# Performance work log

Hardware: AMD Instinct MI355X
Metric: run time of the kernel (lower is better)

The kernel has to match this reference:

```python
import jax, jax.numpy as jnp
import numpy as np

N_NODES = 100000
N_EDGES = 1600000
B = 256
H = 512
HEADS = 8
DH = H // HEADS


def setup_inputs() -> dict:
    key = jax.random.key(0)
    ks = list(jax.random.split(key, 24))
    def nrm(i, shape, s=0.02):
        return jax.random.normal(ks[i], shape, jnp.float32) * s
    inp = {}
    inp["text_features"] = jax.random.normal(ks[0], (B, 768), jnp.float32)
    inp["video_features"] = jax.random.normal(ks[1], (B, 512), jnp.float32)
    inp["x"] = jax.random.normal(ks[2], (N_NODES, 64), jnp.float32)
    inp["edge_index"] = jax.random.randint(ks[3], (2, N_EDGES), 0, N_NODES, dtype=jnp.int32)
    # sorted node->graph assignment covering all B graphs (no empty segments)
    inp["batch_idx"] = ((jnp.arange(N_NODES) * B) // N_NODES).astype(jnp.int32)
    inp["Wt"] = nrm(4, (768, H)); inp["bt"] = jnp.zeros((H,), jnp.float32)
    inp["Wv"] = nrm(5, (512, H)); inp["bv"] = jnp.zeros((H,), jnp.float32)
    inp["Wq"] = nrm(6, (H, H)); inp["bq"] = jnp.zeros((H,), jnp.float32)
    inp["Wk"] = nrm(7, (H, H)); inp["bk"] = jnp.zeros((H,), jnp.float32)
    inp["Wva"] = nrm(8, (H, H)); inp["bva"] = jnp.zeros((H,), jnp.float32)
    inp["Wo"] = nrm(9, (H, H)); inp["bo"] = jnp.zeros((H,), jnp.float32)
    inp["Wf"] = nrm(10, (2 * H, H)); inp["bf"] = jnp.zeros((H,), jnp.float32)
    inp["G1W"] = nrm(11, (64, 128)); inp["G1b"] = jnp.zeros((128,), jnp.float32)
    inp["G2W"] = nrm(12, (128, 128)); inp["G2b"] = jnp.zeros((128,), jnp.float32)
    inp["G3W"] = nrm(13, (128, 256)); inp["G3b"] = jnp.zeros((256,), jnp.float32)
    inp["Wff"] = nrm(14, (H + 256, H)); inp["bff"] = jnp.zeros((H,), jnp.float32)
    inp["Wb"] = nrm(15, (H, 2)); inp["bb"] = jnp.zeros((2,), jnp.float32)
    inp["Wa"] = nrm(16, (H, 2)); inp["ba"] = jnp.zeros((2,), jnp.float32)
    return inp


def _gcn_conv(h, W, b, src, dst, dis):
    # PyG GCNConv: linear transform, symmetric-normalized aggregation w/ self-loops, bias
    hw = h @ W                                       # [N, C]
    norm = dis[src] * dis[dst]                       # [E]
    msg = hw[src] * norm[:, None]                    # [E, C]
    agg = jax.ops.segment_sum(msg, dst, num_segments=h.shape[0])
    agg = agg + hw * (dis * dis)[:, None]            # self-loop messages
    return agg + b


def reference(text_features, video_features, x, edge_index, batch_idx, Wt, bt, Wv, bv, Wq, bq, Wk, bk, Wva, bva, Wo, bo, Wf, bf, G1W, G1b, G2W, G2b, G3W, G3b, Wff, bff, Wb, bb, Wa, ba):
    # encoders (dropout is eval-mode no-op)
    text_enc = jax.nn.relu(text_features @ Wt + bt)      # [B, H]
    video_enc = jax.nn.relu(video_features @ Wv + bv)    # [B, H]
    # multihead attention; torch seq lens are both 1 (batch acts as N)
    q = (text_enc @ Wq + bq).reshape(B, HEADS, 1, DH)
    k = (video_enc @ Wk + bk).reshape(B, HEADS, 1, DH)
    v = (video_enc @ Wva + bva).reshape(B, HEADS, 1, DH)
    scores = jnp.einsum('bhqd,bhkd->bhqk', q, k) / np.float32(np.sqrt(DH))
    w = jax.nn.softmax(scores, axis=-1)
    attn = jnp.einsum('bhqk,bhkd->bhqd', w, v).reshape(B, H)
    text_attended = attn @ Wo + bo
    # multimodal fusion
    fused = jax.nn.relu(jnp.concatenate([text_attended, video_enc], axis=1) @ Wf + bf)
    # GCN stack
    src, dst = edge_index[0], edge_index[1]
    deg = jax.ops.segment_sum(jnp.ones((N_EDGES,), jnp.float32), dst, num_segments=N_NODES) + 1.0
    dis = jax.lax.rsqrt(deg)
    h = jax.nn.elu(_gcn_conv(x, G1W, G1b, src, dst, dis))
    h = jax.nn.elu(_gcn_conv(h, G2W, G2b, src, dst, dis))
    h = _gcn_conv(h, G3W, G3b, src, dst, dis)            # [N, 256]
    # per-graph mean pooling (the original per-batch Python loop, as one segment-mean)
    counts = jax.ops.segment_sum(jnp.ones((N_NODES,), jnp.float32), batch_idx, num_segments=B)
    pooled = jax.ops.segment_sum(h, batch_idx, num_segments=B) / counts[:, None]  # [B, 256]
    # final fusion + classifier heads
    final = jax.nn.relu(jnp.concatenate([fused, pooled], axis=1) @ Wff + bff)
    bullying = jax.nn.log_softmax(final @ Wb + bb, axis=1)
    aggression = jax.nn.log_softmax(final @ Wa + ba, axis=1)
    return bullying, aggression
```

## Files before the change

### kernel.cpp

```cpp
#include <hip/hip_runtime.h>
#include <hip/hip_bf16.h>

#define N_NODES 100000
#define NPAD    100096
#define N_EDGES 1600000
#define BATCH   256
#define HDIM    512

typedef unsigned short u16;
typedef __attribute__((ext_vector_type(8))) short bf16x8;
typedef __attribute__((ext_vector_type(8))) unsigned short u16x8;
typedef __attribute__((ext_vector_type(4))) float f32x4;

__device__ __forceinline__ float bf2f(u16 u) {
    union { unsigned i; float f; } v; v.i = ((unsigned)u) << 16; return v.f;
}
__device__ __forceinline__ u16 f2bf(float f) {
    __hip_bfloat16 h = __float2bfloat16(f);
    return *reinterpret_cast<u16*>(&h);
}

template<int K, int ACT, int SCALE>
__global__ __launch_bounds__(256) void gemm_mfma(
        const u16* __restrict__ A, const u16* __restrict__ Wt,
        const float* __restrict__ bias, const float* __restrict__ dis,
        u16* __restrict__ C, int N) {
    constexpr int RB = K * 2;
    __shared__ u16 As[128 * K];
    __shared__ u16 Bs[128 * K];
    const int tid  = threadIdx.x;
    const int lane = tid & 63;
    const int w    = tid >> 6;
    const int wr   = w >> 1, wc = w & 1;
    const int row0 = blockIdx.y * 128;
    const int col0 = blockIdx.x * 128;

    constexpr int WB     = 128 * RB / 4;
    constexpr int PASSES = WB / 1024;
    const size_t Abase = (size_t)row0 * K;
    const size_t Bbase = (size_t)col0 * K;
    #pragma unroll
    for (int p = 0; p < PASSES; ++p) {
        int Lb  = w * WB + p * 1024;
        int L   = Lb + lane * 16;
        int row = L / RB;
        int cb  = L % RB;
        int scb = cb ^ ((row & 7) << 4);
        const u16* ga = A  + Abase + (size_t)row * K + (scb >> 1);
        const u16* gb = Wt + Bbase + (size_t)row * K + (scb >> 1);
        __builtin_amdgcn_global_load_lds((const __attribute__((address_space(1))) void*)ga,
            (__attribute__((address_space(3))) void*)&As[Lb >> 1], 16, 0, 0);
        __builtin_amdgcn_global_load_lds((const __attribute__((address_space(1))) void*)gb,
            (__attribute__((address_space(3))) void*)&Bs[Lb >> 1], 16, 0, 0);
    }
    asm volatile("s_waitcnt vmcnt(0)" ::: "memory");
    __syncthreads();

    const int rl = lane & 15;
    const int kg = lane >> 4;
    f32x4 acc[4][4] = {};
    #pragma unroll
    for (int s = 0; s < K / 32; ++s) {
        bf16x8 af[4], bg[4];
        #pragma unroll
        for (int m = 0; m < 4; ++m) {
            int row = wr * 64 + m * 16 + rl;
            int cb  = s * 64 + kg * 16;
            int scb = cb ^ ((row & 7) << 4);
            af[m] = *(const bf16x8*)&As[(row * RB + scb) >> 1];
        }
        #pragma unroll
        for (int n = 0; n < 4; ++n) {
            int row = wc * 64 + n * 16 + rl;
            int cb  = s * 64 + kg * 16;
            int scb = cb ^ ((row & 7) << 4);
            bg[n] = *(const bf16x8*)&Bs[(row * RB + scb) >> 1];
        }
        #pragma unroll
        for (int m = 0; m < 4; ++m)
            #pragma unroll
            for (int n = 0; n < 4; ++n)
                acc[m][n] = __builtin_amdgcn_mfma_f32_16x16x32_bf16(af[m], bg[n], acc[m][n], 0, 0, 0);
    }

    #pragma unroll
    for (int m = 0; m < 4; ++m) {
        #pragma unroll
        for (int r = 0; r < 4; ++r) {
            int grow = row0 + wr * 64 + m * 16 + kg * 4 + r;
            float ds = SCALE ? dis[grow] : 1.f;
            #pragma unroll
            for (int n = 0; n < 4; ++n) {
                int gcol = col0 + wc * 64 + n * 16 + rl;
                float v = acc[m][n][r] + bias[gcol];
                if (ACT == 2) v = v > 0.f ? v : expm1f(v);
                C[(size_t)grow * N + gcol] = f2bf(v * ds);
            }
        }
    }
}

template<int ACT>
__global__ __launch_bounds__(256) void gemm_loop(
        const u16* __restrict__ A, const u16* __restrict__ Wt,
        const float* __restrict__ bias, u16* __restrict__ C,
        int N, int K, int lda, int ldc) {
    __shared__ u16 As[128 * 64];
    __shared__ u16 Bs[128 * 64];
    const int tid  = threadIdx.x;
    const int lane = tid & 63;
    const int w    = tid >> 6;
    const int wr   = w >> 1, wc = w & 1;
    const int row0 = blockIdx.y * 128;
    const int col0 = blockIdx.x * 128;
    const int rl = lane & 15;
    const int kg = lane >> 4;
    f32x4 acc[4][4] = {};

    for (int k0 = 0; k0 < K; k0 += 64) {
        #pragma unroll
        for (int p = 0; p < 4; ++p) {
            int Lb  = w * 4096 + p * 1024;
            int L   = Lb + lane * 16;
            int row = L >> 7;
            int cb  = L & 127;
            int scb = cb ^ ((row & 7) << 4);
            const u16* ga = A  + (size_t)(row0 + row) * lda + k0 + (scb >> 1);
            const u16* gb = Wt + (size_t)(col0 + row) * K   + k0 + (scb >> 1);
            __builtin_amdgcn_global_load_lds((const __attribute__((address_space(1))) void*)ga,
                (__attribute__((address_space(3))) void*)&As[Lb >> 1], 16, 0, 0);
            __builtin_amdgcn_global_load_lds((const __attribute__((address_space(1))) void*)gb,
                (__attribute__((address_space(3))) void*)&Bs[Lb >> 1], 16, 0, 0);
        }
        asm volatile("s_waitcnt vmcnt(0)" ::: "memory");
        __syncthreads();
        #pragma unroll
        for (int s = 0; s < 2; ++s) {
            bf16x8 af[4], bg[4];
            #pragma unroll
            for (int m = 0; m < 4; ++m) {
                int row = wr * 64 + m * 16 + rl;
                int cb  = s * 64 + kg * 16;
                int scb = cb ^ ((row & 7) << 4);
                af[m] = *(const bf16x8*)&As[(row * 128 + scb) >> 1];
            }
            #pragma unroll
            for (int n = 0; n < 4; ++n) {
                int row = wc * 64 + n * 16 + rl;
                int cb  = s * 64 + kg * 16;
                int scb = cb ^ ((row & 7) << 4);
                bg[n] = *(const bf16x8*)&Bs[(row * 128 + scb) >> 1];
            }
            #pragma unroll
            for (int m = 0; m < 4; ++m)
                #pragma unroll
                for (int n = 0; n < 4; ++n)
                    acc[m][n] = __builtin_amdgcn_mfma_f32_16x16x32_bf16(af[m], bg[n], acc[m][n], 0, 0, 0);
        }
        __syncthreads();
    }

    #pragma unroll
    for (int m = 0; m < 4; ++m) {
        #pragma unroll
        for (int r = 0; r < 4; ++r) {
            int grow = row0 + wr * 64 + m * 16 + kg * 4 + r;
            #pragma unroll
            for (int n = 0; n < 4; ++n) {
                int gcol = col0 + wc * 64 + n * 16 + rl;
                float v = acc[m][n][r] + bias[gcol];
                if (ACT == 1) v = fmaxf(v, 0.f);
                C[(size_t)grow * ldc + gcol] = f2bf(v);
            }
        }
    }
}

template<int K, int N>
__device__ __forceinline__ void tw(const float* __restrict__ W, u16* __restrict__ Wt, int t) {
    int n = t / K, k = t - n * K;
    Wt[t] = f2bf(W[(size_t)k * N + n]);
}

__global__ void prep(const float* __restrict__ G1W, u16* __restrict__ g1wt,
                     const float* __restrict__ G2W, u16* __restrict__ g2wt,
                     const float* __restrict__ Wv,  u16* __restrict__ WvT,
                     const float* __restrict__ Wva, u16* __restrict__ WvaT,
                     const float* __restrict__ Wo,  u16* __restrict__ WoT,
                     const float* __restrict__ Wf,  u16* __restrict__ WfT,
                     const float* __restrict__ video, u16* __restrict__ vidbf) {
    const int bid = blockIdx.x, tid = threadIdx.x;
    if (bid < 32)        { tw<64, 128>  (G1W, g1wt, bid * 256 + tid); }
    else if (bid < 96)   { tw<128, 128> (G2W, g2wt, (bid - 32) * 256 + tid); }
    else if (bid < 1120) { tw<512, 512> (Wv,  WvT,  (bid - 96) * 256 + tid); }
    else if (bid < 2144) { tw<512, 512> (Wva, WvaT, (bid - 1120) * 256 + tid); }
    else if (bid < 3168) { tw<512, 512> (Wo,  WoT,  (bid - 2144) * 256 + tid); }
    else if (bid < 5216) { tw<1024, 512>(Wf,  WfT,  (bid - 3168) * 256 + tid); }
    else { int t = (bid - 5216) * 256 + tid; vidbf[t] = f2bf(video[t]); }
}

__global__ void final_fused(const u16* __restrict__ fusedb,
                            const float* __restrict__ pooled, const float* __restrict__ counts,
                            const float* __restrict__ G3W, const float* __restrict__ G3b,
                            const float* __restrict__ Wff, const float* __restrict__ bff,
                            const float* __restrict__ Wb,  const float* __restrict__ bb,
                            const float* __restrict__ Wa,  const float* __restrict__ ba,
                            float* __restrict__ out) {
    __shared__ float cat[768], fin[512], pp[128];
    __shared__ float rd[4][4];
    const int b = blockIdx.x, tid = threadIdx.x;
    cat[tid] = bf2f(fusedb[b * 512 + tid]);
    cat[tid + 256] = bf2f(fusedb[b * 512 + 256 + tid]);
    float inv = 1.f / counts[b];
    if (tid < 128) pp[tid] = pooled[b * 128 + tid] * inv;
    __syncthreads();
    {
        float s = G3b[tid];
        #pragma unroll 8
        for (int k = 0; k < 128; ++k) s += pp[k] * G3W[k * 256 + tid];
        cat[512 + tid] = s;
    }
    __syncthreads();
    {
        float a0 = bff[tid], a1 = bff[tid + 256];
        #pragma unroll 8
        for (int k = 0; k < 768; ++k) {
            float xv = cat[k];
            a0 += xv * Wff[k * 512 + tid];
            a1 += xv * Wff[k * 512 + tid + 256];
        }
        fin[tid] = fmaxf(a0, 0.f);
        fin[tid + 256] = fmaxf(a1, 0.f);
    }
    __syncthreads();
    float z0 = 0.f, z1 = 0.f, y0 = 0.f, y1 = 0.f;
    for (int k = tid; k < 512; k += 256) {
        float f = fin[k];
        z0 += f * Wb[2 * k];
        z1 += f * Wb[2 * k + 1];
        y0 += f * Wa[2 * k];
        y1 += f * Wa[2 * k + 1];
    }
    #pragma unroll
    for (int off = 32; off > 0; off >>= 1) {
        z0 += __shfl_down(z0, off);
        z1 += __shfl_down(z1, off);
        y0 += __shfl_down(y0, off);
        y1 += __shfl_down(y1, off);
    }
    int ww = tid >> 6;
    if ((tid & 63) == 0) { rd[ww][0] = z0; rd[ww][1] = z1; rd[ww][2] = y0; rd[ww][3] = y1; }
    __syncthreads();
    if (tid == 0) {
        float Z0 = rd[0][0] + rd[1][0] + rd[2][0] + rd[3][0] + bb[0];
        float Z1 = rd[0][1] + rd[1][1] + rd[2][1] + rd[3][1] + bb[1];
        float Y0 = rd[0][2] + rd[1][2] + rd[2][2] + rd[3][2] + ba[0];
        float Y1 = rd[0][3] + rd[1][3] + rd[2][3] + rd[3][3] + ba[1];
        float m = fmaxf(Z0, Z1);
        float l = m + logf(expf(Z0 - m) + expf(Z1 - m));
        out[b * 2 + 0] = Z0 - l;
        out[b * 2 + 1] = Z1 - l;
        float m2 = fmaxf(Y0, Y1);
        float l2 = m2 + logf(expf(Y0 - m2) + expf(Y1 - m2));
        out[512 + b * 2 + 0] = Y0 - l2;
        out[512 + b * 2 + 1] = Y1 - l2;
    }
}

__global__ void deg_slot(const int* __restrict__ dstE, int* __restrict__ deg,
                         int* __restrict__ slot, int E) {
    int e = blockIdx.x * blockDim.x + threadIdx.x;
    if (e < E) slot[e] = atomicAdd(&deg[dstE[e]], 1);
}

__global__ void scan1(const int* __restrict__ in, int* __restrict__ out,
                      int* __restrict__ bsum, float* __restrict__ dis, int n) {
    __shared__ int ts[256];
    const int tid = threadIdx.x;
    const int base = blockIdx.x * 1024;
    int v[4];
    #pragma unroll
    for (int i = 0; i < 4; ++i) {
        int idx = base + tid * 4 + i;
        v[i] = (idx < n) ? in[idx] : 0;
        if (idx < NPAD) dis[idx] = rsqrtf((float)v[i] + 1.f);
    }
    ts[tid] = v[0] + v[1] + v[2] + v[3];
    __syncthreads();
    for (int off = 1; off < 256; off <<= 1) {
        int val = (tid >= off) ? ts[tid - off] : 0;
        __syncthreads();
        ts[tid] += val;
        __syncthreads();
    }
    int run = (tid == 0) ? 0 : ts[tid - 1];
    if (tid == 255) bsum[blockIdx.x] = ts[255];
    #pragma unroll
    for (int i = 0; i < 4; ++i) {
        int idx = base + tid * 4 + i;
        if (idx < n) out[idx] = run;
        run += v[i];
    }
}

__global__ void scan2(int* __restrict__ bsum, int nb) {
    int l = threadIdx.x;
    int a = (l < nb) ? bsum[l] : 0;
    int b = (l + 64 < nb) ? bsum[l + 64] : 0;
    int oa = a, ob = b;
    #pragma unroll
    for (int off = 1; off < 64; off <<= 1) {
        int t = __shfl_up(a, off);
        if (l >= off) a += t;
    }
    int totA = __shfl(a, 63);
    #pragma unroll
    for (int off = 1; off < 64; off <<= 1) {
        int t = __shfl_up(b, off);
        if (l >= off) b += t;
    }
    if (l < nb) bsum[l] = a - oa;
    if (l + 64 < nb) bsum[l + 64] = totA + b - ob;
}

__global__ void scan3(int* __restrict__ out, const int* __restrict__ bsum, int n, int total) {
    int idx = blockIdx.x * 1024 + threadIdx.x * 4;
    int add = bsum[blockIdx.x];
    #pragma unroll
    for (int i = 0; i < 4; ++i)
        if (idx + i < n) out[idx + i] += add;
    if (blockIdx.x == 0 && threadIdx.x == 0) out[n] = total;
}

__global__ void csr_scatter2(const int* __restrict__ srcE, const int* __restrict__ dstE,
                             const int* __restrict__ rowptr, const int* __restrict__ slot,
                             int* __restrict__ csr_src, int E) {
    int e = blockIdx.x * blockDim.x + threadIdx.x;
    if (e >= E) return;
    csr_src[rowptr[dstE[e]] + slot[e]] = srcE[e];
}

__global__ void scale_rows64_bf16(const float* __restrict__ x, const float* __restrict__ dis,
                                  u16* __restrict__ out) {
    int t = blockIdx.x * blockDim.x + threadIdx.x;
    if (t >= N_NODES * 64) return;
    out[t] = f2bf(x[t] * dis[t >> 6]);
}

template<int C>
__global__ void csr_agg_bf16(const u16* __restrict__ Hs, const int* __restrict__ rowptr,
                             const int* __restrict__ csr_src, const float* __restrict__ dis,
                             u16* __restrict__ out) {
    constexpr int LPG = C / 8;
    constexpr int G   = 64 / LPG;
    int node = blockIdx.x * 4 + (threadIdx.x >> 6);
    if (node >= N_NODES) return;
    int lane = threadIdx.x & 63;
    int g  = lane / LPG;
    int cl = lane % LPG;
    int s0 = rowptr[node], s1 = rowptr[node + 1];
    float a[8] = {};
    if (g == 0) {
        u16x8 v = *(const u16x8*)&Hs[(size_t)node * C + cl * 8];
        #pragma unroll
        for (int j = 0; j < 8; ++j) a[j] = bf2f(v[j]);
    }
    int e = s0 + g;
    while (e + G < s1) {
        int sA = csr_src[e], sB = csr_src[e + G];
        u16x8 vA = *(const u16x8*)&Hs[(size_t)sA * C + cl * 8];
        u16x8 vB = *(const u16x8*)&Hs[(size_t)sB * C + cl * 8];
        #pragma unroll
        for (int j = 0; j < 8; ++j) a[j] += bf2f(vA[j]) + bf2f(vB[j]);
        e += 2 * G;
    }
    while (e < s1) {
        int s = csr_src[e];
        u16x8 v = *(const u16x8*)&Hs[(size_t)s * C + cl * 8];
        #pragma unroll
        for (int j = 0; j < 8; ++j) a[j] += bf2f(v[j]);
        e += G;
    }
    #pragma unroll
    for (int m = LPG; m < 64; m <<= 1)
        #pragma unroll
        for (int j = 0; j < 8; ++j) a[j] += __shfl_xor(a[j], m);
    if (g == 0) {
        float dd = dis[node];
        u16x8 o;
        #pragma unroll
        for (int j = 0; j < 8; ++j) o[j] = f2bf(a[j] * dd);
        *(u16x8*)&out[(size_t)node * C + cl * 8] = o;
    }
}

__global__ __launch_bounds__(256) void csr_agg_pool(
        const u16* __restrict__ Hs, const int* __restrict__ rowptr,
        const int* __restrict__ csr_src, const float* __restrict__ dis,
        const int* __restrict__ batch,
        float* __restrict__ pooled, float* __restrict__ counts) {
    __shared__ float bins[2][128];
    __shared__ int cnt[2];
    const int tid = threadIdx.x;
    const int base = blockIdx.x * 16;
    if (tid < 128) { bins[0][tid] = 0.f; bins[1][tid] = 0.f; }
    if (tid < 2) cnt[tid] = 0;
    __syncthreads();
    const int lane = tid & 63;
    const int w = tid >> 6;
    const int g = lane >> 4;
    const int cl = lane & 15;
    const int b0 = batch[base];
    #pragma unroll
    for (int i = 0; i < 4; ++i) {
        const int node = base + w * 4 + i;
        const int s0 = rowptr[node], s1 = rowptr[node + 1];
        float a[8] = {};
        if (g == 0) {
            u16x8 v = *(const u16x8*)&Hs[(size_t)node * 128 + cl * 8];
            #pragma unroll
            for (int j = 0; j < 8; ++j) a[j] = bf2f(v[j]);
        }
        int e = s0 + g;
        while (e + 4 < s1) {
            int sA = csr_src[e], sB = csr_src[e + 4];
            u16x8 vA = *(const u16x8*)&Hs[(size_t)sA * 128 + cl * 8];
            u16x8 vB = *(const u16x8*)&Hs[(size_t)sB * 128 + cl * 8];
            #pragma unroll
            for (int j = 0; j < 8; ++j) a[j] += bf2f(vA[j]) + bf2f(vB[j]);
            e += 8;
        }
        while (e < s1) {
            int s = csr_src[e];
            u16x8 v = *(const u16x8*)&Hs[(size_t)s * 128 + cl * 8];
            #pragma unroll
            for (int j = 0; j < 8; ++j) a[j] += bf2f(v[j]);
            e += 4;
        }
        #pragma unroll
        for (int m = 16; m < 64; m <<= 1)
            #pragma unroll
            for (int j = 0; j < 8; ++j) a[j] += __shfl_xor(a[j], m);
        if (g == 0) {
            int bin = (batch[node] != b0) ? 1 : 0;
            float dd = dis[node];
            #pragma unroll
            for (int j = 0; j < 8; ++j) atomicAdd(&bins[bin][cl * 8 + j], a[j] * dd);
            if (cl == 0) atomicAdd(&cnt[bin], 1);
        }
    }
    __syncthreads();
    int bin = tid >> 7, c = tid & 127;
    if (cnt[bin] > 0) atomicAdd(&pooled[(b0 + bin) * 128 + c], bins[bin][c]);
    if (tid < 2 && cnt[tid] > 0) atomicAdd(&counts[b0 + tid], (float)cnt[tid]);
}

extern "C" void kernel_launch(void* const* d_in, const int* in_sizes, int n_in,
                              void* d_out, int out_size, void* d_ws, size_t ws_size,
                              hipStream_t stream) {
    const float* video = (const float*)d_in[1];
    const float* x     = (const float*)d_in[2];
    const int*   eidx  = (const int*)d_in[3];
    const int*   batch = (const int*)d_in[4];
    const float* Wv  = (const float*)d_in[7],  *bv  = (const float*)d_in[8];
    const float* Wva = (const float*)d_in[13], *bva = (const float*)d_in[14];
    const float* Wo  = (const float*)d_in[15], *bo  = (const float*)d_in[16];
    const float* Wf  = (const float*)d_in[17], *bf  = (const float*)d_in[18];
    const float* G1W = (const float*)d_in[19], *G1b = (const float*)d_in[20];
    const float* G2W = (const float*)d_in[21], *G2b = (const float*)d_in[22];
    const float* G3W = (const float*)d_in[23], *G3b = (const float*)d_in[24];
    const float* Wff = (const float*)d_in[25], *bff = (const float*)d_in[26];
    const float* Wb  = (const float*)d_in[27], *bb  = (const float*)d_in[28];
    const float* Wa  = (const float*)d_in[29], *ba  = (const float*)d_in[30];
    const int* srcE = eidx;
    const int* dstE = eidx + N_EDGES;

    char* wsc = (char*)d_ws;
    size_t off = 0;
    auto alloc = [&](size_t bytes) { char* p = wsc + off; off += (bytes + 255) & ~(size_t)255; return p; };
    u16*   bufA   = (u16*)  alloc((size_t)NPAD * 128 * 2);
    u16*   bufB   = (u16*)  alloc((size_t)NPAD * 128 * 2);
    float* dis    = (float*)alloc(NPAD * 4);
    int*   deg    = (int*)  alloc(NPAD * 4);
    int*   rowptr = (int*)  alloc((N_NODES + 1) * 4);
    int*   slot   = (int*)  alloc((size_t)N_EDGES * 4);
    int*   csrsrc = (int*)  alloc((size_t)N_EDGES * 4);
    int*   bsum   = (int*)  alloc(128 * 4);
    u16*   g1wt   = (u16*)  alloc(128 * 64 * 2);
    u16*   g2wt   = (u16*)  alloc(128 * 128 * 2);
    u16*   WvT    = (u16*)  alloc(512 * 512 * 2);
    u16*   WvaT   = (u16*)  alloc(512 * 512 * 2);
    u16*   WoT    = (u16*)  alloc(512 * 512 * 2);
    u16*   WfT    = (u16*)  alloc(512 * 1024 * 2);
    u16*   vidbf  = (u16*)  alloc(BATCH * 512 * 2);
    u16*   catb   = (u16*)  alloc(BATCH * 1024 * 2);
    u16*   vattnb = (u16*)  alloc(BATCH * 512 * 2);
    u16*   fusedb = (u16*)  alloc(BATCH * 512 * 2);
    float* pooled = (float*)alloc((BATCH * 128 + BATCH) * 4);
    float* counts = pooled + BATCH * 128;

    const int NB = (N_NODES + 1023) / 1024;
    const int aggGrid = (N_NODES + 3) / 4;

    hipMemsetAsync(deg, 0, NPAD * 4, stream);
    hipMemsetAsync(pooled, 0, (BATCH * 128 + BATCH) * 4, stream);
    deg_slot<<<(N_EDGES + 255) / 256, 256, 0, stream>>>(dstE, deg, slot, N_EDGES);
    scan1<<<NB, 256, 0, stream>>>(deg, rowptr, bsum, dis, N_NODES);
    scan2<<<1, 64, 0, stream>>>(bsum, NB);
    scan3<<<NB, 256, 0, stream>>>(rowptr, bsum, N_NODES, N_EDGES);
    csr_scatter2<<<(N_EDGES + 255) / 256, 256, 0, stream>>>(srcE, dstE, rowptr, slot, csrsrc, N_EDGES);

    prep<<<5728, 256, 0, stream>>>(G1W, g1wt, G2W, g2wt, Wv, WvT, Wva, WvaT,
                                   Wo, WoT, Wf, WfT, video, vidbf);

    dim3 feGrid(4, 2);
    gemm_loop<1><<<feGrid, 256, 0, stream>>>(vidbf, WvT, bv, catb + 512, 512, 512, 512, 1024);
    gemm_loop<0><<<feGrid, 256, 0, stream>>>(catb + 512, WvaT, bva, vattnb, 512, 512, 1024, 512);
    gemm_loop<0><<<feGrid, 256, 0, stream>>>(vattnb, WoT, bo, catb, 512, 512, 512, 1024);
    gemm_loop<1><<<feGrid, 256, 0, stream>>>(catb, WfT, bf, fusedb, 512, 1024, 1024, 512);

    scale_rows64_bf16<<<(N_NODES * 64 + 255) / 256, 256, 0, stream>>>(x, dis, bufA);
    csr_agg_bf16<64><<<aggGrid, 256, 0, stream>>>(bufA, rowptr, csrsrc, dis, bufB);
    gemm_mfma<64, 2, 1><<<dim3(1, NPAD / 128), 256, 0, stream>>>(bufB, g1wt, G1b, dis, bufA, 128);
    csr_agg_bf16<128><<<aggGrid, 256, 0, stream>>>(bufA, rowptr, csrsrc, dis, bufB);
    gemm_mfma<128, 2, 1><<<dim3(1, NPAD / 128), 256, 0, stream>>>(bufB, g2wt, G2b, dis, bufA, 128);
    csr_agg_pool<<<N_NODES / 16, 256, 0, stream>>>(bufA, rowptr, csrsrc, dis, batch, pooled, counts);

    final_fused<<<BATCH, 256, 0, stream>>>(fusedb, pooled, counts, G3W, G3b,
                                           Wff, bff, Wb, bb, Wa, ba, (float*)d_out);
}
```

Baseline: 478.2 us.

## Split 128-wide aggregation across two waves and shrink dense GEMM tiles

The 128-channel CSR aggregation and the pooling aggregation now split each node's channels into two 64-wide halves handled by separate waves. Each wave has 8 edge groups instead of 4, so more neighbour gathers are in flight per node and the cross-lane reduction is shallower. The small batch GEMMs use 64x64 tiles in place of 128x128 to launch 32 blocks instead of 8, filling more compute units. The cost is that node index and rowptr loads are duplicated per half, and the smaller GEMM tiles reuse each loaded tile less.

```diff
diff --git a/kernel.cpp b/kernel.cpp
--- a/kernel.cpp
+++ b/kernel.cpp
@@ -101,26 +101,26 @@
 }
 
 template<int ACT>
-__global__ __launch_bounds__(256) void gemm_loop(
+__global__ __launch_bounds__(256) void gemm64(
         const u16* __restrict__ A, const u16* __restrict__ Wt,
         const float* __restrict__ bias, u16* __restrict__ C,
-        int N, int K, int lda, int ldc) {
-    __shared__ u16 As[128 * 64];
-    __shared__ u16 Bs[128 * 64];
+        int K, int lda, int ldc) {
+    __shared__ u16 As[64 * 64];
+    __shared__ u16 Bs[64 * 64];
     const int tid  = threadIdx.x;
     const int lane = tid & 63;
     const int w    = tid >> 6;
     const int wr   = w >> 1, wc = w & 1;
-    const int row0 = blockIdx.y * 128;
-    const int col0 = blockIdx.x * 128;
+    const int row0 = blockIdx.y * 64;
+    const int col0 = blockIdx.x * 64;
     const int rl = lane & 15;
     const int kg = lane >> 4;
-    f32x4 acc[4][4] = {};
+    f32x4 acc[2][2] = {};
 
     for (int k0 = 0; k0 < K; k0 += 64) {
         #pragma unroll
-        for (int p = 0; p < 4; ++p) {
-            int Lb  = w * 4096 + p * 1024;
+        for (int p = 0; p < 2; ++p) {
+            int Lb  = w * 2048 + p * 1024;
             int L   = Lb + lane * 16;
             int row = L >> 7;
             int cb  = L & 127;
@@ -136,38 +136,38 @@
         __syncthreads();
         #pragma unroll
         for (int s = 0; s < 2; ++s) {
-            bf16x8 af[4], bg[4];
-            #pragma unroll
-            for (int m = 0; m < 4; ++m) {
-                int row = wr * 64 + m * 16 + rl;
+            bf16x8 af[2], bg[2];
+            #pragma unroll
+            for (int m = 0; m < 2; ++m) {
+                int row = wr * 32 + m * 16 + rl;
                 int cb  = s * 64 + kg * 16;
                 int scb = cb ^ ((row & 7) << 4);
                 af[m] = *(const bf16x8*)&As[(row * 128 + scb) >> 1];
             }
             #pragma unroll
-            for (int n = 0; n < 4; ++n) {
-                int row = wc * 64 + n * 16 + rl;
+            for (int n = 0; n < 2; ++n) {
+                int row = wc * 32 + n * 16 + rl;
                 int cb  = s * 64 + kg * 16;
                 int scb = cb ^ ((row & 7) << 4);
                 bg[n] = *(const bf16x8*)&Bs[(row * 128 + scb) >> 1];
             }
             #pragma unroll
-            for (int m = 0; m < 4; ++m)
+            for (int m = 0; m < 2; ++m)
                 #pragma unroll
-                for (int n = 0; n < 4; ++n)
+                for (int n = 0; n < 2; ++n)
                     acc[m][n] = __builtin_amdgcn_mfma_f32_16x16x32_bf16(af[m], bg[n], acc[m][n], 0, 0, 0);
         }
         __syncthreads();
     }
 
     #pragma unroll
-    for (int m = 0; m < 4; ++m) {
+    for (int m = 0; m < 2; ++m) {
         #pragma unroll
         for (int r = 0; r < 4; ++r) {
-            int grow = row0 + wr * 64 + m * 16 + kg * 4 + r;
-            #pragma unroll
-            for (int n = 0; n < 4; ++n) {
-                int gcol = col0 + wc * 64 + n * 16 + rl;
+            int grow = row0 + wr * 32 + m * 16 + kg * 4 + r;
+            #pragma unroll
+            for (int n = 0; n < 2; ++n) {
+                int gcol = col0 + wc * 32 + n * 16 + rl;
                 float v = acc[m][n][r] + bias[gcol];
                 if (ACT == 1) v = fmaxf(v, 0.f);
                 C[(size_t)grow * ldc + gcol] = f2bf(v);
@@ -347,42 +347,39 @@
     out[t] = f2bf(x[t] * dis[t >> 6]);
 }
 
-template<int C>
-__global__ void csr_agg_bf16(const u16* __restrict__ Hs, const int* __restrict__ rowptr,
-                             const int* __restrict__ csr_src, const float* __restrict__ dis,
-                             u16* __restrict__ out) {
-    constexpr int LPG = C / 8;
-    constexpr int G   = 64 / LPG;
+__global__ void csr_agg64(const u16* __restrict__ Hs, const int* __restrict__ rowptr,
+                          const int* __restrict__ csr_src, const float* __restrict__ dis,
+                          u16* __restrict__ out) {
     int node = blockIdx.x * 4 + (threadIdx.x >> 6);
     if (node >= N_NODES) return;
     int lane = threadIdx.x & 63;
-    int g  = lane / LPG;
-    int cl = lane % LPG;
+    int g  = lane >> 3;
+    int cl = lane & 7;
     int s0 = rowptr[node], s1 = rowptr[node + 1];
     float a[8] = {};
     if (g == 0) {
-        u16x8 v = *(const u16x8*)&Hs[(size_t)node * C + cl * 8];
+        u16x8 v = *(const u16x8*)&Hs[(size_t)node * 64 + cl * 8];
         #pragma unroll
         for (int j = 0; j < 8; ++j) a[j] = bf2f(v[j]);
     }
     int e = s0 + g;
-    while (e + G < s1) {
-        int sA = csr_src[e], sB = csr_src[e + G];
-        u16x8 vA = *(const u16x8*)&Hs[(size_t)sA * C + cl * 8];
-        u16x8 vB = *(const u16x8*)&Hs[(size_t)sB * C + cl * 8];
+    while (e + 8 < s1) {
+        int sA = csr_src[e], sB = csr_src[e + 8];
+        u16x8 vA = *(const u16x8*)&Hs[(size_t)sA * 64 + cl * 8];
+        u16x8 vB = *(const u16x8*)&Hs[(size_t)sB * 64 + cl * 8];
         #pragma unroll
         for (int j = 0; j < 8; ++j) a[j] += bf2f(vA[j]) + bf2f(vB[j]);
-        e += 2 * G;
+        e += 16;
     }
     while (e < s1) {
         int s = csr_src[e];
-        u16x8 v = *(const u16x8*)&Hs[(size_t)s * C + cl * 8];
+        u16x8 v = *(const u16x8*)&Hs[(size_t)s * 64 + cl * 8];
         #pragma unroll
         for (int j = 0; j < 8; ++j) a[j] += bf2f(v[j]);
-        e += G;
-    }
-    #pragma unroll
-    for (int m = LPG; m < 64; m <<= 1)
+        e += 8;
+    }
+    #pragma unroll
+    for (int m = 8; m < 64; m <<= 1)
         #pragma unroll
         for (int j = 0; j < 8; ++j) a[j] += __shfl_xor(a[j], m);
     if (g == 0) {
@@ -390,7 +387,55 @@
         u16x8 o;
         #pragma unroll
         for (int j = 0; j < 8; ++j) o[j] = f2bf(a[j] * dd);
-        *(u16x8*)&out[(size_t)node * C + cl * 8] = o;
+        *(u16x8*)&out[(size_t)node * 64 + cl * 8] = o;
+    }
+}
+
+__global__ __launch_bounds__(256) void csr_agg128_split(
+        const u16* __restrict__ Hs, const int* __restrict__ rowptr,
+        const int* __restrict__ csr_src, const float* __restrict__ dis,
+        u16* __restrict__ out) {
+    const int tid  = threadIdx.x;
+    const int w    = tid >> 6;
+    const int lane = tid & 63;
+    const int node = blockIdx.x * 2 + (w >> 1);
+    const int half = w & 1;
+    const int g  = lane >> 3;
+    const int cl = lane & 7;
+    const int coff = half * 64 + cl * 8;
+    const int s0 = rowptr[node], s1 = rowptr[node + 1];
+    float a[8] = {};
+    if (g == 0) {
+        u16x8 v = *(const u16x8*)&Hs[(size_t)node * 128 + coff];
+        #pragma unroll
+        for (int j = 0; j < 8; ++j) a[j] = bf2f(v[j]);
+    }
+    int e = s0 + g;
+    while (e + 8 < s1) {
+        int sA = csr_src[e], sB = csr_src[e + 8];
+        u16x8 vA = *(const u16x8*)&Hs[(size_t)sA * 128 + coff];
+        u16x8 vB = *(const u16x8*)&Hs[(size_t)sB * 128 + coff];
+        #pragma unroll
+        for (int j = 0; j < 8; ++j) a[j] += bf2f(vA[j]) + bf2f(vB[j]);
+        e += 16;
+    }
+    while (e < s1) {
+        int s = csr_src[e];
+        u16x8 v = *(const u16x8*)&Hs[(size_t)s * 128 + coff];
+        #pragma unroll
+        for (int j = 0; j < 8; ++j) a[j] += bf2f(v[j]);
+        e += 8;
+    }
+    #pragma unroll
+    for (int m = 8; m < 64; m <<= 1)
+        #pragma unroll
+        for (int j = 0; j < 8; ++j) a[j] += __shfl_xor(a[j], m);
+    if (g == 0) {
+        float dd = dis[node];
+        u16x8 o;
+        #pragma unroll
+        for (int j = 0; j < 8; ++j) o[j] = f2bf(a[j] * dd);
+        *(u16x8*)&out[(size_t)node * 128 + coff] = o;
     }
 }
 
@@ -406,47 +451,50 @@
     if (tid < 128) { bins[0][tid] = 0.f; bins[1][tid] = 0.f; }
     if (tid < 2) cnt[tid] = 0;
     __syncthreads();
+    const int w    = tid >> 6;
     const int lane = tid & 63;
-    const int w = tid >> 6;
-    const int g = lane >> 4;
-    const int cl = lane & 15;
+    const int g  = lane >> 3;
+    const int cl = lane & 7;
     const int b0 = batch[base];
     #pragma unroll
-    for (int i = 0; i < 4; ++i) {
-        const int node = base + w * 4 + i;
+    for (int i = 0; i < 8; ++i) {
+        const int T    = w * 8 + i;
+        const int node = base + (T >> 1);
+        const int half = T & 1;
+        const int coff = half * 64 + cl * 8;
         const int s0 = rowptr[node], s1 = rowptr[node + 1];
         float a[8] = {};
         if (g == 0) {
-            u16x8 v = *(const u16x8*)&Hs[(size_t)node * 128 + cl * 8];
+            u16x8 v = *(const u16x8*)&Hs[(size_t)node * 128 + coff];
             #pragma unroll
             for (int j = 0; j < 8; ++j) a[j] = bf2f(v[j]);
         }
         int e = s0 + g;
-        while (e + 4 < s1) {
-            int sA = csr_src[e], sB = csr_src[e + 4];
-            u16x8 vA = *(const u16x8*)&Hs[(size_t)sA * 128 + cl * 8];
-            u16x8 vB = *(const u16x8*)&Hs[(size_t)sB * 128 + cl * 8];
+        while (e + 8 < s1) {
+            int sA = csr_src[e], sB = csr_src[e + 8];
+            u16x8 vA = *(const u16x8*)&Hs[(size_t)sA * 128 + coff];
+            u16x8 vB = *(const u16x8*)&Hs[(size_t)sB * 128 + coff];
             #pragma unroll
             for (int j = 0; j < 8; ++j) a[j] += bf2f(vA[j]) + bf2f(vB[j]);
-            e += 8;
+            e += 16;
         }
         while (e < s1) {
             int s = csr_src[e];
-            u16x8 v = *(const u16x8*)&Hs[(size_t)s * 128 + cl * 8];
+            u16x8 v = *(const u16x8*)&Hs[(size_t)s * 128 + coff];
             #pragma unroll
             for (int j = 0; j < 8; ++j) a[j] += bf2f(v[j]);
-            e += 4;
-        }
-        #pragma unroll
-        for (int m = 16; m < 64; m <<= 1)
+            e += 8;
+        }
+        #pragma unroll
+        for (int m = 8; m < 64; m <<= 1)
             #pragma unroll
             for (int j = 0; j < 8; ++j) a[j] += __shfl_xor(a[j], m);
         if (g == 0) {
             int bin = (batch[node] != b0) ? 1 : 0;
             float dd = dis[node];
             #pragma unroll
-            for (int j = 0; j < 8; ++j) atomicAdd(&bins[bin][cl * 8 + j], a[j] * dd);
-            if (cl == 0) atomicAdd(&cnt[bin], 1);
+            for (int j = 0; j < 8; ++j) atomicAdd(&bins[bin][coff + j], a[j] * dd);
+            if (cl == 0 && half == 0) atomicAdd(&cnt[bin], 1);
         }
     }
     __syncthreads();
@@ -500,7 +548,6 @@
     float* counts = pooled + BATCH * 128;
 
     const int NB = (N_NODES + 1023) / 1024;
-    const int aggGrid = (N_NODES + 3) / 4;
 
     hipMemsetAsync(deg, 0, NPAD * 4, stream);
     hipMemsetAsync(pooled, 0, (BATCH * 128 + BATCH) * 4, stream);
@@ -513,16 +560,16 @@
     prep<<<5728, 256, 0, stream>>>(G1W, g1wt, G2W, g2wt, Wv, WvT, Wva, WvaT,
                                    Wo, WoT, Wf, WfT, video, vidbf);
 
-    dim3 feGrid(4, 2);
-    gemm_loop<1><<<feGrid, 256, 0, stream>>>(vidbf, WvT, bv, catb + 512, 512, 512, 512, 1024);
-    gemm_loop<0><<<feGrid, 256, 0, stream>>>(catb + 512, WvaT, bva, vattnb, 512, 512, 1024, 512);
-    gemm_loop<0><<<feGrid, 256, 0, stream>>>(vattnb, WoT, bo, catb, 512, 512, 512, 1024);
-    gemm_loop<1><<<feGrid, 256, 0, stream>>>(catb, WfT, bf, fusedb, 512, 1024, 1024, 512);
+    dim3 fe512(8, 4);
+    gemm64<1><<<fe512, 256, 0, stream>>>(vidbf, WvT, bv, catb + 512, 512, 512, 1024);
+    gemm64<0><<<fe512, 256, 0, stream>>>(catb + 512, WvaT, bva, vattnb, 512, 1024, 512);
+    gemm64<0><<<fe512, 256, 0, stream>>>(vattnb, WoT, bo, catb, 512, 512, 1024);
+    gemm64<1><<<fe512, 256, 0, stream>>>(catb, WfT, bf, fusedb, 1024, 1024, 512);
 
     scale_rows64_bf16<<<(N_NODES * 64 + 255) / 256, 256, 0, stream>>>(x, dis, bufA);
-    csr_agg_bf16<64><<<aggGrid, 256, 0, stream>>>(bufA, rowptr, csrsrc, dis, bufB);
+    csr_agg64<<<(N_NODES + 3) / 4, 256, 0, stream>>>(bufA, rowptr, csrsrc, dis, bufB);
     gemm_mfma<64, 2, 1><<<dim3(1, NPAD / 128), 256, 0, stream>>>(bufB, g1wt, G1b, dis, bufA, 128);
-    csr_agg_bf16<128><<<aggGrid, 256, 0, stream>>>(bufA, rowptr, csrsrc, dis, bufB);
+    csr_agg128_split<<<N_NODES / 2, 256, 0, stream>>>(bufA, rowptr, csrsrc, dis, bufB);
     gemm_mfma<128, 2, 1><<<dim3(1, NPAD / 128), 256, 0, stream>>>(bufB, g2wt, G2b, dis, bufA, 128);
     csr_agg_pool<<<N_NODES / 16, 256, 0, stream>>>(bufA, rowptr, csrsrc, dis, batch, pooled, counts);
 
```

After: 504.5 us. +5.5%, slower.
